# Performance work log

Measured on AMD Instinct MI355X. Metric: run time of the kernel, lower is better.

Reference implementation:

```python
import jax, jax.numpy as jnp
import numpy as np

LATENT_DIM = 256
NUM_CODEBOOKS = 8
CODEBOOK_SIZE = 512
SUB_DIM = LATENT_DIM // NUM_CODEBOOKS
COMMIT_W = 0.25
CODEBOOK_W = 1.0


def setup_inputs() -> dict:
    key = jax.random.key(0)
    k1, k2 = jax.random.split(key)
    latents = jax.random.normal(k1, (16, 4096, LATENT_DIM), dtype=jnp.float32)
    patch_mask = jnp.ones((16, 4096), dtype=jnp.float32)
    bound = 1.0 / CODEBOOK_SIZE
    codebooks = jax.random.uniform(
        k2, (NUM_CODEBOOKS, CODEBOOK_SIZE, SUB_DIM),
        minval=-bound, maxval=bound, dtype=jnp.float32)
    return {"latents": latents, "patch_mask": patch_mask, "codebooks": codebooks}


def reference(latents, patch_mask, codebooks):
    B, N, D = latents.shape
    C, K, d = codebooks.shape
    x = latents.reshape(B, N, C, d)  # split per codebook

    # squared L2 distances to every codebook entry: (B, N, C, K)
    dist = ((x ** 2).sum(-1, keepdims=True)
            + (codebooks ** 2).sum(-1)[None, None]
            - 2.0 * jnp.einsum('bncd,ckd->bnck', x, codebooks))
    ids = jnp.argmin(dist, axis=-1)  # (B, N, C) int

    # gather nearest entries: (B, N, C, d)
    quant = codebooks[jnp.arange(C)[None, None, :], ids]

    # mse_loss is a mean over equal-sized tensors per codebook, so the mean of
    # per-codebook means equals one global mean
    commitment_loss = jnp.mean((x - jax.lax.stop_gradient(quant)) ** 2) * COMMIT_W
    codebook_loss = jnp.mean((quant - jax.lax.stop_gradient(x)) ** 2) * CODEBOOK_W

    # perplexity over active (masked) patches, per codebook then averaged
    one_hot = jax.nn.one_hot(ids, K, dtype=latents.dtype)  # (B, N, C, K)
    denom = jnp.maximum(patch_mask.sum(), 1.0)
    avg_probs = jnp.einsum('bnck,bn->ck', one_hot, patch_mask) / denom
    perplexity = jnp.mean(jnp.exp(-(avg_probs * jnp.log(avg_probs + 1e-8)).sum(-1)))

    quant_flat = quant.reshape(B, N, D)
    st_quantized = latents + jax.lax.stop_gradient(quant_flat - latents)
    return ids, quant_flat, st_quantized, commitment_loss, codebook_loss, perplexity
```

## Files before the change

### kernel.cpp

```cpp
#include <hip/hip_runtime.h>
#include <math.h>

#define BB 16
#define NN 4096
#define DD 256
#define CC 8
#define KK 512
#define SD 32
#define NTOK (BB * NN)
#define IDS_N (NTOK * CC)
#define QN (NTOK * DD)
#define OFF_Q   (IDS_N)
#define OFF_ST  (IDS_N + QN)
#define OFF_SC  (IDS_N + 2 * QN)

#define GUARD 6e-5f
#define CAP 65536

#define WS_ZERO (32 + 16384)

typedef float f32x4 __attribute__((ext_vector_type(4)));
typedef short s16x8 __attribute__((ext_vector_type(8)));

__device__ __forceinline__ unsigned short f2bf(float f) {
    unsigned u = __float_as_uint(f);
    u += 0x7fffu + ((u >> 16) & 1u);
    return (unsigned short)(u >> 16);
}
__device__ __forceinline__ float bf2f(unsigned short h) {
    return __uint_as_float(((unsigned)h) << 16);
}
__device__ __forceinline__ void split8(const float4 a, const float4 b,
                                       s16x8& hv, s16x8& lv) {
    unsigned short h;
    h = f2bf(a.x); hv[0]=(short)h; lv[0]=(short)f2bf(a.x - bf2f(h));
    h = f2bf(a.y); hv[1]=(short)h; lv[1]=(short)f2bf(a.y - bf2f(h));
    h = f2bf(a.z); hv[2]=(short)h; lv[2]=(short)f2bf(a.z - bf2f(h));
    h = f2bf(a.w); hv[3]=(short)h; lv[3]=(short)f2bf(a.w - bf2f(h));
    h = f2bf(b.x); hv[4]=(short)h; lv[4]=(short)f2bf(b.x - bf2f(h));
    h = f2bf(b.y); hv[5]=(short)h; lv[5]=(short)f2bf(b.y - bf2f(h));
    h = f2bf(b.z); hv[6]=(short)h; lv[6]=(short)f2bf(b.z - bf2f(h));
    h = f2bf(b.w); hv[7]=(short)h; lv[7]=(short)f2bf(b.w - bf2f(h));
}

__global__ __launch_bounds__(256) void vq_prep(
    const float* __restrict__ cbs, const float* __restrict__ mask,
    float* __restrict__ csqf, double* __restrict__ mask_sum)
{
    __shared__ double red[256];
    const int tid = threadIdx.x;
    const int cell = blockIdx.x * 256 + tid;
    const float* cp = cbs + (size_t)cell * SD;
    double s = 0.0;
    #pragma unroll
    for (int j = 0; j < 8; ++j) {
        float4 v = ((const float4*)cp)[j];
        double a = (double)v.x, b = (double)v.y, c = (double)v.z, d = (double)v.w;
        s = fma(a, a, s); s = fma(b, b, s);
        s = fma(c, c, s); s = fma(d, d, s);
    }
    csqf[cell] = (float)s;

    double m = 0.0;
    for (int i = cell; i < NTOK; i += 4096) m += (double)mask[i];
    red[tid] = m;
    __syncthreads();
    for (int st = 128; st > 0; st >>= 1) {
        if (tid < st) red[tid] += red[tid + st];
        __syncthreads();
    }
    if (tid == 0) atomicAdd(mask_sum, red[0]);
}

__global__ __launch_bounds__(512, 4) void vq_score(
    const float* __restrict__ latents, const float* __restrict__ mask,
    const float* __restrict__ cbs, const float* __restrict__ csq_g,
    float* __restrict__ out, double* __restrict__ mse_sum,
    float* __restrict__ hist, unsigned* __restrict__ count,
    unsigned* __restrict__ list)
{
    __shared__ unsigned short s_hi[KK * SD];
    __shared__ unsigned short s_lo[KK * SD];
    __shared__ float  s_csq[KK];
    __shared__ float  s_lhist[KK];
    __shared__ float  s_best[8][32];
    __shared__ float  s_sec[8][32];
    __shared__ int    s_bid[8][32];
    __shared__ double s_mse[8];

    const int tid = threadIdx.x;
    const int c   = blockIdx.x & 7;
    const int tb  = blockIdx.x >> 3;

    {
        const int cw = tid;
        const float* cp = cbs + ((size_t)c * KK + cw) * SD;
        s_csq[cw] = csq_g[c * KK + cw];
        s_lhist[cw] = 0.f;
        const int sw = (cw >> 1) & 3;
        #pragma unroll
        for (int q = 0; q < 4; ++q) {
            float4 a = ((const float4*)cp)[2 * q];
            float4 b = ((const float4*)cp)[2 * q + 1];
            s16x8 hv, lv;
            split8(a, b, hv, lv);
            ((s16x8*)(s_hi + (size_t)cw * SD))[q ^ sw] = hv;
            ((s16x8*)(s_lo + (size_t)cw * SD))[q ^ sw] = lv;
        }
    }
    __syncthreads();

    const int wv   = tid >> 6;
    const int lane = tid & 63;
    const int col  = lane & 15;
    const int kb   = lane >> 4;

    double mseTot = 0.0;

    #pragma unroll 1
    for (int p = 0; p < 4; ++p) {
        const int tok0 = tb * 1024 + p * 256 + wv * 32;

        s16x8 ah[2], al[2];
        #pragma unroll
        for (int t = 0; t < 2; ++t) {
            const int token = tok0 + t * 16 + col;
            const float4* xp =
                (const float4*)(latents + (size_t)token * DD + c * SD + kb * 8);
            split8(xp[0], xp[1], ah[t], al[t]);
        }

        float best[2][4], sec[2][4]; int bid[2][4];
        #pragma unroll
        for (int t = 0; t < 2; ++t)
            #pragma unroll
            for (int r = 0; r < 4; ++r) {
                best[t][r] = 1e30f; sec[t][r] = 1e30f; bid[t][r] = 0;
            }

        for (int nt = 0; nt < 32; ++nt) {
            const int kcol = nt * 16 + col;
            const int slot = kb ^ ((kcol >> 1) & 3);
            const float cs = s_csq[kcol];
            const s16x8 bh = *((const s16x8*)(s_hi + (size_t)kcol * SD + slot * 8));
            const s16x8 bl = *((const s16x8*)(s_lo + (size_t)kcol * SD + slot * 8));
            #pragma unroll
            for (int t = 0; t < 2; ++t) {
                f32x4 acc = {0.f, 0.f, 0.f, 0.f};
                acc = __builtin_amdgcn_mfma_f32_16x16x32_bf16(ah[t], bh, acc, 0, 0, 0);
                acc = __builtin_amdgcn_mfma_f32_16x16x32_bf16(ah[t], bl, acc, 0, 0, 0);
                acc = __builtin_amdgcn_mfma_f32_16x16x32_bf16(al[t], bh, acc, 0, 0, 0);
                #pragma unroll
                for (int r = 0; r < 4; ++r) {
                    const float s = fmaf(-2.f, acc[r], cs);
                    const bool lt = s < best[t][r];
                    bid[t][r]  = lt ? kcol : bid[t][r];
                    sec[t][r]  = __builtin_amdgcn_fmed3f(s, best[t][r], sec[t][r]);
                    best[t][r] = fminf(best[t][r], s);
                }
            }
        }

        #pragma unroll
        for (int m = 1; m <= 8; m <<= 1) {
            #pragma unroll
            for (int t = 0; t < 2; ++t)
                #pragma unroll
                for (int r = 0; r < 4; ++r) {
                    const float ob = __shfl_xor(best[t][r], m, 64);
                    const float os = __shfl_xor(sec[t][r],  m, 64);
                    const int   oi = __shfl_xor(bid[t][r],  m, 64);
                    const float ns = fminf(fmaxf(best[t][r], ob),
                                           fminf(sec[t][r], os));
                    const bool tk = (ob < best[t][r]) ||
                                    (ob == best[t][r] && oi < bid[t][r]);
                    bid[t][r]  = tk ? oi : bid[t][r];
                    best[t][r] = fminf(best[t][r], ob);
                    sec[t][r]  = ns;
                }
        }

        asm volatile("s_waitcnt lgkmcnt(0)" ::: "memory");
        if (col == 0) {
            #pragma unroll
            for (int t = 0; t < 2; ++t)
                #pragma unroll
                for (int r = 0; r < 4; ++r) {
                    const int idx = t * 16 + kb * 4 + r;
                    s_best[wv][idx] = best[t][r];
                    s_sec[wv][idx]  = sec[t][r];
                    s_bid[wv][idx]  = bid[t][r];
                }
        }
        asm volatile("s_waitcnt lgkmcnt(0)" ::: "memory");

        const int tl    = lane >> 1;
        const int half  = lane & 1;
        const int token = tok0 + tl;
        const float bb  = s_best[wv][tl];
        const float ssv = s_sec[wv][tl];
        const int   bi  = s_bid[wv][tl];
        const bool flag = (ssv - bb) < GUARD;

        const float* qp = cbs + ((size_t)c * KK + bi) * SD + half * 16;
        const float* xp = latents + (size_t)token * DD + c * SD + half * 16;
        float* oq  = out + OFF_Q  + (size_t)token * DD + c * SD + half * 16;
        float* ost = out + OFF_ST + (size_t)token * DD + c * SD + half * 16;
        double acc = 0.0;
        #pragma unroll
        for (int j = 0; j < 4; ++j) {
            float4 qv = ((const float4*)qp)[j];
            float4 xv = ((const float4*)xp)[j];
            float4 sv;
            sv.x = xv.x + (qv.x - xv.x);
            sv.y = xv.y + (qv.y - xv.y);
            sv.z = xv.z + (qv.z - xv.z);
            sv.w = xv.w + (qv.w - xv.w);
            double d;
            d = (double)xv.x - (double)qv.x; acc = fma(d, d, acc);
            d = (double)xv.y - (double)qv.y; acc = fma(d, d, acc);
            d = (double)xv.z - (double)qv.z; acc = fma(d, d, acc);
            d = (double)xv.w - (double)qv.w; acc = fma(d, d, acc);
            ((float4*)oq)[j]  = qv;
            ((float4*)ost)[j] = sv;
        }
        if (!flag) mseTot += acc;
        if (half == 0) {
            out[(size_t)token * CC + c] = (float)bi;
            if (!flag) {
                atomicAdd(&s_lhist[bi], mask[token]);
            } else {
                unsigned slot = atomicAdd(count, 1u);
                if (slot < CAP) list[slot] = ((unsigned)token << 3) | (unsigned)c;
            }
        }
    }

    #pragma unroll
    for (int off = 32; off > 0; off >>= 1)
        mseTot += __shfl_down(mseTot, off, 64);
    if (lane == 0) s_mse[wv] = mseTot;
    __syncthreads();
    if (tid == 0) {
        double s = 0.0;
        #pragma unroll
        for (int w = 0; w < 8; ++w) s += s_mse[w];
        atomicAdd(mse_sum, s);
    }
    {
        float v = s_lhist[tid];
        if (v != 0.f) atomicAdd(&hist[c * KK + tid], v);
    }
}

__global__ __launch_bounds__(256, 2) void vq_resolve(
    const float* __restrict__ latents, const float* __restrict__ mask,
    const float* __restrict__ cbs, const float* __restrict__ csq_g,
    float* __restrict__ out, double* __restrict__ mse_sum,
    float* __restrict__ hist, const unsigned* __restrict__ count,
    const unsigned* __restrict__ list)
{
    unsigned n = *count; if (n > CAP) n = CAP;
    const int lane  = threadIdx.x & 63;
    const int wave  = (blockIdx.x << 2) | (threadIdx.x >> 6);
    const int nwav  = gridDim.x << 2;

    for (unsigned i = wave; i < n; i += nwav) {
        const unsigned e = list[i];
        const int token = (int)(e >> 3), c = (int)(e & 7u);
        const float* xp = latents + (size_t)token * DD + c * SD;

        float4 xv[8];
        #pragma unroll
        for (int j = 0; j < 8; ++j) xv[j] = ((const float4*)xp)[j];

        double xs = 0.0;
        #pragma unroll
        for (int j = 0; j < 8; ++j) {
            xs = fma((double)xv[j].x, (double)xv[j].x, xs);
            xs = fma((double)xv[j].y, (double)xv[j].y, xs);
            xs = fma((double)xv[j].z, (double)xv[j].z, xs);
            xs = fma((double)xv[j].w, (double)xv[j].w, xs);
        }
        const float xsqf = (float)xs;
        const float* cbase = cbs + (size_t)c * KK * SD;
        const float* csqc  = csq_g + c * KK;

        float best = 1e30f; int bk = lane * 8;
        #pragma unroll
        for (int j = 0; j < 8; ++j) {
            const int k = lane * 8 + j;
            const float4* cw = (const float4*)(cbase + k * SD);
            double d0 = 0.0, d1 = 0.0, d2 = 0.0, d3 = 0.0;
            #pragma unroll
            for (int q = 0; q < 8; ++q) {
                float4 cv = cw[q];
                d0 = fma((double)cv.x, (double)xv[q].x, d0);
                d1 = fma((double)cv.y, (double)xv[q].y, d1);
                d2 = fma((double)cv.z, (double)xv[q].z, d2);
                d3 = fma((double)cv.w, (double)xv[q].w, d3);
            }
            const float dotf = (float)((d0 + d1) + (d2 + d3));
            const float t1 = xsqf + csqc[k];
            const float dist = t1 - 2.0f * dotf;
            if (dist < best) { best = dist; bk = k; }
        }
        #pragma unroll
        for (int off = 32; off > 0; off >>= 1) {
            float od = __shfl_down(best, off, 64);
            int   ok = __shfl_down(bk,   off, 64);
            if (od < best || (od == best && ok < bk)) { best = od; bk = ok; }
        }
        bk = __shfl(bk, 0, 64);

        const int oldid = (int)out[(size_t)token * CC + c];
        if (bk != oldid) {
            if (lane == 0) out[(size_t)token * CC + c] = (float)bk;
            if (lane < SD) {
                float q = cbase[bk * SD + lane];
                float x = xp[lane];
                out[OFF_Q  + (size_t)token * DD + c * SD + lane] = q;
                out[OFF_ST + (size_t)token * DD + c * SD + lane] = x + (q - x);
            }
        }
        double dd = 0.0;
        if (lane < SD) {
            double q = (double)cbase[bk * SD + lane];
            double df = (double)xp[lane] - q;
            dd = df * df;
        }
        #pragma unroll
        for (int off = 32; off > 0; off >>= 1) dd += __shfl_down(dd, off, 64);
        if (lane == 0) {
            atomicAdd(mse_sum, dd);
            atomicAdd(&hist[c * KK + bk], mask[token]);
        }
    }
}

__global__ __launch_bounds__(512) void vq_final(
    const float* __restrict__ hist, const double* __restrict__ mse_sum,
    const double* __restrict__ mask_sum, float* __restrict__ out)
{
    __shared__ double ent[CC];
    const int tid = threadIdx.x;
    double denom = *mask_sum; if (denom < 1.0) denom = 1.0;

    const int w = tid >> 6;
    const int lane = tid & 63;
    double t = 0.0;
    for (int k = lane; k < KK; k += 64) {
        double p = (double)hist[w * KK + k] / denom;
        t += p * log(p + 1e-8);
    }
    #pragma unroll
    for (int off = 32; off > 0; off >>= 1) t += __shfl_down(t, off, 64);
    if (lane == 0) ent[w] = -t;
    __syncthreads();

    if (tid == 0) {
        double mean = mse_sum[0] / (double)QN;
        out[OFF_SC + 0] = (float)(0.25 * mean);
        out[OFF_SC + 1] = (float)(1.0 * mean);
        double perp = 0.0;
        for (int cc = 0; cc < CC; ++cc) perp += exp(ent[cc]);
        out[OFF_SC + 2] = (float)(perp / (double)CC);
    }
}

extern "C" void kernel_launch(void* const* d_in, const int* in_sizes, int n_in,
                              void* d_out, int out_size, void* d_ws, size_t ws_size,
                              hipStream_t stream) {
    const float* latents = (const float*)d_in[0];
    const float* mask    = (const float*)d_in[1];
    const float* cbs     = (const float*)d_in[2];
    float* out = (float*)d_out;

    double*   mse      = (double*)d_ws;
    double*   mask_sum = (double*)((char*)d_ws + 8);
    unsigned* count    = (unsigned*)((char*)d_ws + 16);
    float*    hist     = (float*)((char*)d_ws + 32);
    float*    csqf     = (float*)((char*)d_ws + 32 + 16384);
    unsigned* list     = (unsigned*)((char*)d_ws + 32 + 32768);

    hipMemsetAsync(d_ws, 0, WS_ZERO, stream);

    vq_prep<<<dim3(16), dim3(256), 0, stream>>>(cbs, mask, csqf, mask_sum);
    vq_score<<<dim3(512), dim3(512), 0, stream>>>(
        latents, mask, cbs, csqf, out, mse, hist, count, list);
    vq_resolve<<<dim3(2048), dim3(256), 0, stream>>>(
        latents, mask, cbs, csqf, out, mse, hist, count, list);
    vq_final<<<dim3(1), dim3(512), 0, stream>>>(hist, mse, mask_sum, out);
}
```

Before: 410.4 us.

## Move quant/ST emission to separate kernel, prefetch latents, lane-parallel resolve

The quantized and straight-through output writes and the MSE accumulation move out of the score and resolve kernels into a new full-token emit kernel that runs after ids are final. Because quant is now written once, the conditional rewrite in resolve goes away. The score kernel prefetches the next pass's latents while it processes the current one. The resolve kernel splits each dot product across 8 lanes with xor-shuffle reductions instead of 8 entries per lane holding a whole row. The cost is an extra kernel launch and a second read of latents and ids from global memory.

After: 348.5 us. -15.1%, faster.

```diff
diff --git a/kernel.cpp b/kernel.cpp
--- a/kernel.cpp
+++ b/kernel.cpp
@@ -75,9 +75,8 @@
 __global__ __launch_bounds__(512, 4) void vq_score(
     const float* __restrict__ latents, const float* __restrict__ mask,
     const float* __restrict__ cbs, const float* __restrict__ csq_g,
-    float* __restrict__ out, double* __restrict__ mse_sum,
-    float* __restrict__ hist, unsigned* __restrict__ count,
-    unsigned* __restrict__ list)
+    float* __restrict__ out, float* __restrict__ hist,
+    unsigned* __restrict__ count, unsigned* __restrict__ list)
 {
     __shared__ unsigned short s_hi[KK * SD];
     __shared__ unsigned short s_lo[KK * SD];
@@ -86,7 +85,6 @@
     __shared__ float  s_best[8][32];
     __shared__ float  s_sec[8][32];
     __shared__ int    s_bid[8][32];
-    __shared__ double s_mse[8];
 
     const int tid = threadIdx.x;
     const int c   = blockIdx.x & 7;
@@ -115,7 +113,14 @@
     const int col  = lane & 15;
     const int kb   = lane >> 4;
 
-    double mseTot = 0.0;
+    float4 xa[2][2];
+    #pragma unroll
+    for (int t = 0; t < 2; ++t) {
+        const int token = tb * 1024 + wv * 32 + t * 16 + col;
+        const float4* xp =
+            (const float4*)(latents + (size_t)token * DD + c * SD + kb * 8);
+        xa[t][0] = xp[0]; xa[t][1] = xp[1];
+    }
 
     #pragma unroll 1
     for (int p = 0; p < 4; ++p) {
@@ -123,11 +128,16 @@
 
         s16x8 ah[2], al[2];
         #pragma unroll
-        for (int t = 0; t < 2; ++t) {
-            const int token = tok0 + t * 16 + col;
-            const float4* xp =
-                (const float4*)(latents + (size_t)token * DD + c * SD + kb * 8);
-            split8(xp[0], xp[1], ah[t], al[t]);
+        for (int t = 0; t < 2; ++t) split8(xa[t][0], xa[t][1], ah[t], al[t]);
+
+        if (p < 3) {
+            #pragma unroll
+            for (int t = 0; t < 2; ++t) {
+                const int token = tb * 1024 + (p + 1) * 256 + wv * 32 + t * 16 + col;
+                const float4* xp =
+                    (const float4*)(latents + (size_t)token * DD + c * SD + kb * 8);
+                xa[t][0] = xp[0]; xa[t][1] = xp[1];
+            }
         }
 
         float best[2][4], sec[2][4]; int bid[2][4];
@@ -194,38 +204,12 @@
         }
         asm volatile("s_waitcnt lgkmcnt(0)" ::: "memory");
 
-        const int tl    = lane >> 1;
-        const int half  = lane & 1;
-        const int token = tok0 + tl;
-        const float bb  = s_best[wv][tl];
-        const float ssv = s_sec[wv][tl];
-        const int   bi  = s_bid[wv][tl];
-        const bool flag = (ssv - bb) < GUARD;
-
-        const float* qp = cbs + ((size_t)c * KK + bi) * SD + half * 16;
-        const float* xp = latents + (size_t)token * DD + c * SD + half * 16;
-        float* oq  = out + OFF_Q  + (size_t)token * DD + c * SD + half * 16;
-        float* ost = out + OFF_ST + (size_t)token * DD + c * SD + half * 16;
-        double acc = 0.0;
-        #pragma unroll
-        for (int j = 0; j < 4; ++j) {
-            float4 qv = ((const float4*)qp)[j];
-            float4 xv = ((const float4*)xp)[j];
-            float4 sv;
-            sv.x = xv.x + (qv.x - xv.x);
-            sv.y = xv.y + (qv.y - xv.y);
-            sv.z = xv.z + (qv.z - xv.z);
-            sv.w = xv.w + (qv.w - xv.w);
-            double d;
-            d = (double)xv.x - (double)qv.x; acc = fma(d, d, acc);
-            d = (double)xv.y - (double)qv.y; acc = fma(d, d, acc);
-            d = (double)xv.z - (double)qv.z; acc = fma(d, d, acc);
-            d = (double)xv.w - (double)qv.w; acc = fma(d, d, acc);
-            ((float4*)oq)[j]  = qv;
-            ((float4*)ost)[j] = sv;
-        }
-        if (!flag) mseTot += acc;
-        if (half == 0) {
+        if (lane < 32) {
+            const int token = tok0 + lane;
+            const float bb  = s_best[wv][lane];
+            const float ssv = s_sec[wv][lane];
+            const int   bi  = s_bid[wv][lane];
+            const bool flag = (ssv - bb) < GUARD;
             out[(size_t)token * CC + c] = (float)bi;
             if (!flag) {
                 atomicAdd(&s_lhist[bi], mask[token]);
@@ -236,106 +220,108 @@
         }
     }
 
-    #pragma unroll
-    for (int off = 32; off > 0; off >>= 1)
-        mseTot += __shfl_down(mseTot, off, 64);
-    if (lane == 0) s_mse[wv] = mseTot;
-    __syncthreads();
-    if (tid == 0) {
-        double s = 0.0;
-        #pragma unroll
-        for (int w = 0; w < 8; ++w) s += s_mse[w];
-        atomicAdd(mse_sum, s);
-    }
+    __syncthreads();
     {
         float v = s_lhist[tid];
         if (v != 0.f) atomicAdd(&hist[c * KK + tid], v);
     }
 }
 
-__global__ __launch_bounds__(256, 2) void vq_resolve(
+__global__ __launch_bounds__(256) void vq_resolve(
     const float* __restrict__ latents, const float* __restrict__ mask,
     const float* __restrict__ cbs, const float* __restrict__ csq_g,
-    float* __restrict__ out, double* __restrict__ mse_sum,
-    float* __restrict__ hist, const unsigned* __restrict__ count,
-    const unsigned* __restrict__ list)
+    float* __restrict__ out, float* __restrict__ hist,
+    const unsigned* __restrict__ count, const unsigned* __restrict__ list)
 {
     unsigned n = *count; if (n > CAP) n = CAP;
-    const int lane  = threadIdx.x & 63;
-    const int wave  = (blockIdx.x << 2) | (threadIdx.x >> 6);
-    const int nwav  = gridDim.x << 2;
+    const int lane = threadIdx.x & 63;
+    const int wave = (blockIdx.x << 2) | (threadIdx.x >> 6);
+    const int nwav = gridDim.x << 2;
+    const int dq = lane & 7;
+    const int kk = lane >> 3;
 
     for (unsigned i = wave; i < n; i += nwav) {
         const unsigned e = list[i];
         const int token = (int)(e >> 3), c = (int)(e & 7u);
         const float* xp = latents + (size_t)token * DD + c * SD;
 
-        float4 xv[8];
-        #pragma unroll
-        for (int j = 0; j < 8; ++j) xv[j] = ((const float4*)xp)[j];
-
-        double xs = 0.0;
-        #pragma unroll
-        for (int j = 0; j < 8; ++j) {
-            xs = fma((double)xv[j].x, (double)xv[j].x, xs);
-            xs = fma((double)xv[j].y, (double)xv[j].y, xs);
-            xs = fma((double)xv[j].z, (double)xv[j].z, xs);
-            xs = fma((double)xv[j].w, (double)xv[j].w, xs);
-        }
-        const float xsqf = (float)xs;
+        const float4 xq = ((const float4*)xp)[dq];
+        const double x0 = (double)xq.x, x1 = (double)xq.y;
+        const double x2 = (double)xq.z, x3 = (double)xq.w;
+
+        double px = fma(x3, x3, fma(x2, x2, fma(x1, x1, x0 * x0)));
+        px += __shfl_xor(px, 1, 64);
+        px += __shfl_xor(px, 2, 64);
+        px += __shfl_xor(px, 4, 64);
+        const float xsqf = (float)px;
+
         const float* cbase = cbs + (size_t)c * KK * SD;
         const float* csqc  = csq_g + c * KK;
 
-        float best = 1e30f; int bk = lane * 8;
-        #pragma unroll
-        for (int j = 0; j < 8; ++j) {
-            const int k = lane * 8 + j;
-            const float4* cw = (const float4*)(cbase + k * SD);
-            double d0 = 0.0, d1 = 0.0, d2 = 0.0, d3 = 0.0;
-            #pragma unroll
-            for (int q = 0; q < 8; ++q) {
-                float4 cv = cw[q];
-                d0 = fma((double)cv.x, (double)xv[q].x, d0);
-                d1 = fma((double)cv.y, (double)xv[q].y, d1);
-                d2 = fma((double)cv.z, (double)xv[q].z, d2);
-                d3 = fma((double)cv.w, (double)xv[q].w, d3);
-            }
-            const float dotf = (float)((d0 + d1) + (d2 + d3));
+        float best = 1e30f; int bk = kk;
+        #pragma unroll 4
+        for (int jk = 0; jk < 64; ++jk) {
+            const int k = jk * 8 + kk;
+            const float4 cv = ((const float4*)(cbase + (size_t)k * SD))[dq];
+            double d = fma((double)cv.w, x3, fma((double)cv.z, x2,
+                       fma((double)cv.y, x1, (double)cv.x * x0)));
+            d += __shfl_xor(d, 1, 64);
+            d += __shfl_xor(d, 2, 64);
+            d += __shfl_xor(d, 4, 64);
+            const float dotf = (float)d;
             const float t1 = xsqf + csqc[k];
             const float dist = t1 - 2.0f * dotf;
             if (dist < best) { best = dist; bk = k; }
         }
         #pragma unroll
-        for (int off = 32; off > 0; off >>= 1) {
-            float od = __shfl_down(best, off, 64);
-            int   ok = __shfl_down(bk,   off, 64);
+        for (int m = 8; m <= 32; m <<= 1) {
+            const float od = __shfl_xor(best, m, 64);
+            const int   ok = __shfl_xor(bk,   m, 64);
             if (od < best || (od == best && ok < bk)) { best = od; bk = ok; }
         }
-        bk = __shfl(bk, 0, 64);
-
-        const int oldid = (int)out[(size_t)token * CC + c];
-        if (bk != oldid) {
-            if (lane == 0) out[(size_t)token * CC + c] = (float)bk;
-            if (lane < SD) {
-                float q = cbase[bk * SD + lane];
-                float x = xp[lane];
-                out[OFF_Q  + (size_t)token * DD + c * SD + lane] = q;
-                out[OFF_ST + (size_t)token * DD + c * SD + lane] = x + (q - x);
-            }
-        }
-        double dd = 0.0;
-        if (lane < SD) {
-            double q = (double)cbase[bk * SD + lane];
-            double df = (double)xp[lane] - q;
-            dd = df * df;
-        }
-        #pragma unroll
-        for (int off = 32; off > 0; off >>= 1) dd += __shfl_down(dd, off, 64);
         if (lane == 0) {
-            atomicAdd(mse_sum, dd);
+            out[(size_t)token * CC + c] = (float)bk;
             atomicAdd(&hist[c * KK + bk], mask[token]);
         }
     }
+}
+
+__global__ __launch_bounds__(256) void vq_emit(
+    const float* __restrict__ latents, const float* __restrict__ cbs,
+    float* __restrict__ out, double* __restrict__ mse_sum)
+{
+    __shared__ double s_red[4];
+    const int tid  = threadIdx.x;
+    const int lane = tid & 63;
+    const int wv   = tid >> 6;
+    const int c    = lane >> 3;
+    const int dq   = lane & 7;
+    const int wave = blockIdx.x * 4 + wv;
+
+    double acc = 0.0;
+    for (int token = wave; token < NTOK; token += 8192) {
+        const int bi = (int)out[(size_t)token * CC + c];
+        const float4 xq = ((const float4*)(latents + (size_t)token * DD))[lane];
+        const float4 qv = ((const float4*)(cbs + ((size_t)c * KK + bi) * SD))[dq];
+        float4 sv;
+        sv.x = xq.x + (qv.x - xq.x);
+        sv.y = xq.y + (qv.y - xq.y);
+        sv.z = xq.z + (qv.z - xq.z);
+        sv.w = xq.w + (qv.w - xq.w);
+        ((float4*)(out + OFF_Q  + (size_t)token * DD))[lane] = qv;
+        ((float4*)(out + OFF_ST + (size_t)token * DD))[lane] = sv;
+        double d;
+        d = (double)xq.x - (double)qv.x; acc = fma(d, d, acc);
+        d = (double)xq.y - (double)qv.y; acc = fma(d, d, acc);
+        d = (double)xq.z - (double)qv.z; acc = fma(d, d, acc);
+        d = (double)xq.w - (double)qv.w; acc = fma(d, d, acc);
+    }
+    #pragma unroll
+    for (int off = 32; off > 0; off >>= 1) acc += __shfl_down(acc, off, 64);
+    if (lane == 0) s_red[wv] = acc;
+    __syncthreads();
+    if (tid == 0)
+        atomicAdd(mse_sum, s_red[0] + s_red[1] + s_red[2] + s_red[3]);
 }
 
 __global__ __launch_bounds__(512) void vq_final(
@@ -387,8 +373,9 @@
 
     vq_prep<<<dim3(16), dim3(256), 0, stream>>>(cbs, mask, csqf, mask_sum);
     vq_score<<<dim3(512), dim3(512), 0, stream>>>(
-        latents, mask, cbs, csqf, out, mse, hist, count, list);
+        latents, mask, cbs, csqf, out, hist, count, list);
     vq_resolve<<<dim3(2048), dim3(256), 0, stream>>>(
-        latents, mask, cbs, csqf, out, mse, hist, count, list);
+        latents, mask, cbs, csqf, out, hist, count, list);
+    vq_emit<<<dim3(2048), dim3(256), 0, stream>>>(latents, cbs, out, mse);
     vq_final<<<dim3(1), dim3(512), 0, stream>>>(hist, mse, mask_sum, out);
 }
```
